# Kernel tuning notes

Measured on AMD Instinct MI355X. Metric: run time of the kernel, lower is better.

Reference implementation:

```python
import jax, jax.numpy as jnp
import numpy as np
from jax import lax

N, CIN, H, W = 4, 1024, 56, 56
CB = 256          # bottleneck channels
K = 9             # 3x3 kernel taps


def _conv(x, w, b, stride=1, padding='SAME'):
    y = lax.conv_general_dilated(x, w, (stride, stride), padding,
                                 dimension_numbers=('NCHW', 'OIHW', 'NCHW'))
    return y + b[None, :, None, None]


def _bilinear_gather(feat, ys, xs):
    # feat: [N,C,H,W]; ys, xs: [N,P] float sample coords. Zero padding outside.
    n, c, h, w = feat.shape
    y0 = jnp.floor(ys); x0 = jnp.floor(xs)
    wy1 = ys - y0; wy0 = 1.0 - wy1
    wx1 = xs - x0; wx0 = 1.0 - wx1
    flat = feat.reshape(n, c, h * w)

    def g(yi, xi):
        valid = (yi >= 0) & (yi <= h - 1) & (xi >= 0) & (xi <= w - 1)
        yc = jnp.clip(yi, 0, h - 1).astype(jnp.int32)
        xc = jnp.clip(xi, 0, w - 1).astype(jnp.int32)
        idx = (yc * w + xc)  # [N,P]
        vals = jnp.take_along_axis(flat, idx[:, None, :], axis=2)  # [N,C,P]
        return vals * valid[:, None, :].astype(feat.dtype)

    out = (g(y0, x0) * (wy0 * wx0)[:, None, :]
           + g(y0, x0 + 1) * (wy0 * wx1)[:, None, :]
           + g(y0 + 1, x0) * (wy1 * wx0)[:, None, :]
           + g(y0 + 1, x0 + 1) * (wy1 * wx1)[:, None, :])
    return out  # [N,C,P]


def _deform_conv3x3(feat, w, b, w_off, b_off):
    # DCNv1: offsets predicted by a standard 3x3 conv (18 = 2*K channels),
    # then bilinear-sample input at p + p_k + offset, accumulate with kernel w.
    n, c, h, ww = feat.shape
    off = _conv(feat, w_off, b_off)                 # [N, 2K, H, W]
    off = off.reshape(n, K, 2, h, ww)
    dy, dx = off[:, :, 0], off[:, :, 1]             # [N,K,H,W]
    ki, kj = jnp.meshgrid(jnp.arange(3), jnp.arange(3), indexing='ij')
    ky = (ki.reshape(-1) - 1).astype(feat.dtype)    # kernel dy offsets, rate=1
    kx = (kj.reshape(-1) - 1).astype(feat.dtype)
    hh = jnp.arange(h, dtype=feat.dtype)
    wc = jnp.arange(ww, dtype=feat.dtype)
    ys = hh[None, None, :, None] + ky[None, :, None, None] + dy   # [N,K,H,W]
    xs = wc[None, None, None, :] + kx[None, :, None, None] + dx
    sampled = _bilinear_gather(feat, ys.reshape(n, -1), xs.reshape(n, -1))
    sampled = sampled.reshape(n, c, K, h, ww)       # [N,C,K,H,W]
    out = jnp.einsum('nckhw,ock->nohw', sampled, w.reshape(w.shape[0], c, K))
    return out + b[None, :, None, None]


def setup_inputs() -> dict:
    key = jax.random.key(0)
    ks = jax.random.split(key, 6)
    x = jax.random.normal(ks[0], (N, CIN, H, W), dtype=jnp.float32)
    w1 = jax.random.normal(ks[1], (CB, CIN, 1, 1), dtype=jnp.float32) * 0.02
    b1 = jnp.zeros((CB,), jnp.float32)
    w_off = jax.random.normal(ks[2], (2 * K, CB, 3, 3), dtype=jnp.float32) * 0.01
    b_off = jnp.zeros((2 * K,), jnp.float32)
    w2 = jax.random.normal(ks[3], (CB, CB, 3, 3), dtype=jnp.float32) * 0.02
    b2 = jnp.zeros((CB,), jnp.float32)
    w3 = jax.random.normal(ks[4], (CIN, CB, 1, 1), dtype=jnp.float32) * 0.02
    b3 = jnp.zeros((CIN,), jnp.float32)
    return {"x": x, "w1": w1, "b1": b1, "w_off": w_off, "b_off": b_off,
            "w2": w2, "b2": b2, "w3": w3, "b3": b3}


def reference(x, w1, b1, w_off, b_off, w2, b2, w3, b3):
    # shortcut is identity (in_channels == out_channels, stride=1)
    r = jax.nn.relu(_conv(x, w1, b1))                      # conv1 1x1 + relu
    r = jax.nn.relu(_deform_conv3x3(r, w2, b2, w_off, b_off))  # deform 3x3 + relu
    r = _conv(r, w3, b3)                                   # conv3 1x1, no act
    return jax.nn.relu(x + r)
```

## Files before the change

kernel.cpp:

```cpp
#include <hip/hip_runtime.h>
#include <hip/hip_bf16.h>

#define N_   4
#define CIN  1024
#define H_   56
#define W_   56
#define HW   3136
#define CB   256
#define KK   9
#define OFFC 18

typedef __attribute__((ext_vector_type(8))) short short8;
typedef __attribute__((ext_vector_type(4))) short short4v;
typedef __attribute__((ext_vector_type(4))) float float4v;
typedef unsigned short ushort_t;

__device__ inline ushort_t bf16_rne(float f) {
    unsigned int u = __float_as_uint(f);
    unsigned int r = (u + 0x7FFFu + ((u >> 16) & 1u)) >> 16;
    return (ushort_t)r;
}
__device__ inline void split_bf16(float f, ushort_t& hi, ushort_t& lo) {
    ushort_t h = bf16_rne(f);
    float hf = __uint_as_float(((unsigned int)h) << 16);
    hi = h;
    lo = bf16_rne(f - hf);
}
__device__ inline short8 ld_frag_lds(const ushort_t* base) {
    short4v a = *(const short4v*)base;
    short4v b = *(const short4v*)(base + 4);
    return __builtin_shufflevector(a, b, 0, 1, 2, 3, 4, 5, 6, 7);
}
__device__ inline void lds_barrier() {
    asm volatile("s_waitcnt lgkmcnt(0)" ::: "memory");
    __builtin_amdgcn_s_barrier();
    __builtin_amdgcn_sched_barrier(0);
}

__global__ void __launch_bounds__(256) pack_weights_kernel(
    const float* __restrict__ w1, const float* __restrict__ w2,
    const float* __restrict__ w3, const float* __restrict__ w_off,
    ushort_t* __restrict__ w1p, ushort_t* __restrict__ w2p,
    ushort_t* __restrict__ w3p, ushort_t* __restrict__ wofp)
{
    int e = blockIdx.x * 256 + threadIdx.x;
    if (e < 256 * 1024) {
        int o = e >> 10, k = e & 1023;
        ushort_t hi, lo; split_bf16(w1[e], hi, lo);
        w1p[(size_t)(o * 2 + 0) * 1024 + k] = hi;
        w1p[(size_t)(o * 2 + 1) * 1024 + k] = lo;
        return;
    }
    e -= 256 * 1024;
    if (e < 256 * 256 * 9) {
        int o = e / 2304; int rem = e % 2304; int c = rem / 9; int k = rem % 9;
        w2p[(size_t)(k * 256 + o) * 256 + c] = bf16_rne(w2[e]);
        return;
    }
    e -= 256 * 256 * 9;
    if (e < 1024 * 256) {
        int o = e >> 8, k = e & 255;
        ushort_t hi, lo; split_bf16(w3[e], hi, lo);
        w3p[(size_t)(o * 2 + 0) * 256 + k] = hi;
        w3p[(size_t)(o * 2 + 1) * 256 + k] = lo;
        return;
    }
    e -= 1024 * 256;
    if (e < 9 * 32 * 256) {
        int k = e / (32 * 256);
        int rem = e % (32 * 256);
        int m = rem >> 8, c = rem & 255;
        float v = (m < OFFC) ? w_off[((size_t)m * 256 + c) * 9 + k] : 0.f;
        wofp[e] = bf16_rne(v);
    }
}

template <int MFRAG, bool RELU, bool RESID>
__global__ void __launch_bounds__(256, 4) conv1x1_mfma_kernel(
    const ushort_t* __restrict__ Wp,
    const float* __restrict__ Xin,
    const float* __restrict__ bias,
    const float* __restrict__ resid,
    float* __restrict__ Cout,
    int M, int Kdim)
{
    __shared__ ushort_t Bs[64][36];

    const int tid  = threadIdx.x;
    const int wave = tid >> 6;
    const int lane = tid & 63;
    const int l15  = lane & 15;
    const int quad = lane >> 4;
    const int pBase = blockIdx.x * 64;
    const int mBase = blockIdx.y * (MFRAG * 64) + wave * (MFRAG * 16);
    const int n     = blockIdx.z;
    const float* Xn = Xin + (size_t)n * Kdim * HW;

    float4v acc[MFRAG][4];
#pragma unroll
    for (int i = 0; i < MFRAG; ++i)
#pragma unroll
        for (int j = 0; j < 4; ++j) acc[i][j] = (float4v)(0.f);

    const int kk = tid >> 3;
    const int pq = (tid & 7) * 8;

    const float* src0 = &Xn[(size_t)kk * HW + pBase + pq];
    float4 c0 = *reinterpret_cast<const float4*>(src0);
    float4 c1 = *reinterpret_cast<const float4*>(src0 + 4);

    for (int k0 = 0; k0 < Kdim; k0 += 32) {
        lds_barrier();
        float vs[8] = {c0.x, c0.y, c0.z, c0.w, c1.x, c1.y, c1.z, c1.w};
#pragma unroll
        for (int j = 0; j < 8; ++j) Bs[pq + j][kk] = bf16_rne(vs[j]);

        short8 ah[MFRAG], al[MFRAG];
#pragma unroll
        for (int mt = 0; mt < MFRAG; ++mt) {
            const ushort_t* arow = Wp +
                ((size_t)(mBase + mt * 16 + l15) * 2) * Kdim + k0 + quad * 8;
            ah[mt] = *(const short8*)(arow);
            al[mt] = *(const short8*)(arow + Kdim);
        }
        if (k0 + 32 < Kdim) {
            const float* src = &Xn[(size_t)(k0 + 32 + kk) * HW + pBase + pq];
            c0 = *reinterpret_cast<const float4*>(src);
            c1 = *reinterpret_cast<const float4*>(src + 4);
        }
        lds_barrier();

        short8 bh[4];
#pragma unroll
        for (int nt = 0; nt < 4; ++nt)
            bh[nt] = ld_frag_lds(&Bs[nt * 16 + l15][quad * 8]);
        __builtin_amdgcn_s_setprio(1);
#pragma unroll
        for (int mt = 0; mt < MFRAG; ++mt)
#pragma unroll
            for (int nt = 0; nt < 4; ++nt) {
                acc[mt][nt] = __builtin_amdgcn_mfma_f32_16x16x32_bf16(
                    ah[mt], bh[nt], acc[mt][nt], 0, 0, 0);
                acc[mt][nt] = __builtin_amdgcn_mfma_f32_16x16x32_bf16(
                    al[mt], bh[nt], acc[mt][nt], 0, 0, 0);
            }
        __builtin_amdgcn_s_setprio(0);
    }

#pragma unroll
    for (int mt = 0; mt < MFRAG; ++mt)
#pragma unroll
        for (int rr = 0; rr < 4; ++rr) {
            int row = mBase + mt * 16 + quad * 4 + rr;
            float bv = bias[row];
#pragma unroll
            for (int nt = 0; nt < 4; ++nt) {
                int col = pBase + nt * 16 + l15;
                size_t idx = ((size_t)n * M + row) * HW + col;
                float v = acc[mt][nt][rr] + bv;
                if (RESID) v += resid[idx];
                if (RELU)  v = fmaxf(v, 0.f);
                Cout[idx] = v;
            }
        }
}

__global__ void __launch_bounds__(256, 2) offset_mfma_kernel(
    const float* __restrict__ r,
    const ushort_t* __restrict__ wofp,
    float* __restrict__ offp)
{
    __shared__ float win[32][174];

    const int tid  = threadIdx.x;
    const int h    = blockIdx.x;
    const int kh   = blockIdx.y;
    const int n    = blockIdx.z;
    const int wave = tid >> 6;
    const int lane = tid & 63;
    const int l15  = lane & 15;
    const int quad = lane >> 4;
    const float* rn = r + (size_t)n * CB * HW;
    const int cb0 = kh * 128;

    const int p = wave * 16 + l15;

    float4v acc[2];
    acc[0] = (float4v)(0.f);
    acc[1] = (float4v)(0.f);

    for (int cb = cb0; cb < cb0 + 128; cb += 32) {
        __syncthreads();
        for (int f = tid; f < 32 * 3 * 14; f += 256) {
            int c = f / 42, remf = f % 42, row = remf / 14, x4 = (remf % 14) * 4;
            int yg = h - 1 + row;
            float4 v = {0.f, 0.f, 0.f, 0.f};
            if (yg >= 0 && yg < H_)
                v = *reinterpret_cast<const float4*>(
                    &rn[(size_t)(cb + c) * HW + yg * W_ + x4]);
            *reinterpret_cast<float4*>(&win[c][row * 56 + x4]) = v;
        }
        __syncthreads();

        short8 ahA0, ahA1, ahB0, ahB1;
        {
            const ushort_t* a0 = wofp + (size_t)(0 * 32 + l15) * 256 + cb + quad * 8;
            ahA0 = *(const short8*)a0;
            ahA1 = *(const short8*)(a0 + 16 * 256);
        }
#pragma unroll
        for (int k = 0; k < KK; ++k) {
            if (k + 1 < KK) {
                const ushort_t* a1 = wofp +
                    (size_t)((k + 1) * 32 + l15) * 256 + cb + quad * 8;
                ahB0 = *(const short8*)a1;
                ahB1 = *(const short8*)(a1 + 16 * 256);
            }
            const int ky = k / 3;
            const int dx = (k % 3) - 1;
            int x = p + dx;
            bool pvalid = (p < 56) && (x >= 0) && (x < 56);
            int xc = min(max(x, 0), 55);
            short8 bh;
#pragma unroll
            for (int j = 0; j < 8; ++j) {
                float v = win[quad * 8 + j][ky * 56 + xc];
                bh[j] = (short)bf16_rne(pvalid ? v : 0.f);
            }
            acc[0] = __builtin_amdgcn_mfma_f32_16x16x32_bf16(
                ahA0, bh, acc[0], 0, 0, 0);
            acc[1] = __builtin_amdgcn_mfma_f32_16x16x32_bf16(
                ahA1, bh, acc[1], 0, 0, 0);
            ahA0 = ahB0; ahA1 = ahB1;
        }
    }

    if (p < 56) {
        float* base = offp + (size_t)(kh * N_ + n) * OFFC * HW;
#pragma unroll
        for (int mt = 0; mt < 2; ++mt)
#pragma unroll
            for (int rr = 0; rr < 4; ++rr) {
                int m = mt * 16 + quad * 4 + rr;
                if (m < OFFC)
                    base[(size_t)m * HW + h * W_ + p] = acc[mt][rr];
            }
    }
}

#define TPX   28
#define WROWS 5
#define WCOLS 36
#define WPOS  (WROWS * WCOLS)
#define CSTR  33
#define WITEMS (32 * WROWS * 9)
#define DBLK  (H_ * 2 * N_)
#define NCHUNK 8

__global__ void __launch_bounds__(512, 2) deform_mfma_kernel(
    const float* __restrict__ r,
    const float* __restrict__ off,
    const float* __restrict__ b_off,
    const ushort_t* __restrict__ w2p,
    const float* __restrict__ b2,
    float* __restrict__ r2)
{
    __shared__ float    win[WPOS][CSTR];
    __shared__ ushort_t Bs[2][KK][32][36];

    const int tid = threadIdx.x;
    const int bid = blockIdx.x;
    const int swz = (bid & 7) * (DBLK >> 3) + (bid >> 3);
    const int xh  = swz & 1;
    const int h   = (swz >> 1) % H_;
    const int n   = swz / (H_ * 2);
    const int xb  = xh * TPX;
    const float* rn    = r + (size_t)n * CB * HW;
    const float* offn0 = off + (size_t)n * OFFC * HW;
    const float* offn1 = off + (size_t)(N_ + n) * OFFC * HW;

    int   bi0 = 0, bi1 = 0, bi2 = 0, bi3 = 0;
    float bw0 = 0.f, bw1 = 0.f, bw2 = 0.f, bw3 = 0.f;
    int   go0 = 0, go1 = 0, go2 = 0, go3 = 0;
    bool  bfast = true;
    const bool bactive = (tid < 288);
    const int  bk = bactive ? (tid / 32) : 0;
    const int  bp = bactive ? (tid % 32) : 0;
    if (bactive && bp < TPX) {
        int pg = xb + bp;
        size_t iy = (size_t)(2 * bk) * HW + h * W_ + pg;
        size_t ix = (size_t)(2 * bk + 1) * HW + h * W_ + pg;
        float dy = offn0[iy] + offn1[iy] + b_off[2 * bk];
        float dx = offn0[ix] + offn1[ix] + b_off[2 * bk + 1];
        float ys = (float)(h + (bk / 3) - 1) + dy;
        float xs = (float)(pg + (bk % 3) - 1) + dx;
        float y0f = floorf(ys), x0f = floorf(xs);
        int y0 = (int)y0f, x0 = (int)x0f;
        float wy1 = ys - y0f, wy0 = 1.f - wy1;
        float wx1 = xs - x0f, wx0 = 1.f - wx1;
        int   wid[4]; float wg[4]; int gof[4]; bool fast = true;
#pragma unroll
        for (int u = 0; u < 2; ++u)
#pragma unroll
            for (int vv = 0; vv < 2; ++vv) {
                int yy = y0 + u, xx = x0 + vv;
                bool valid = (yy >= 0) && (yy <= 55) && (xx >= 0) && (xx <= 55);
                float wgt = valid ? (u ? wy1 : wy0) * (vv ? wx1 : wx0) : 0.f;
                int ry = yy - (h - 2);
                int rx = xx - (xb - 4);
                if (wgt != 0.f &&
                    (ry < 0 || ry >= WROWS || rx < 0 || rx >= WCOLS))
                    fast = false;
                int idx = min(max(ry, 0), WROWS - 1) * WCOLS +
                          min(max(rx, 0), WCOLS - 1);
                wid[u * 2 + vv] = idx;
                wg[u * 2 + vv]  = wgt;
                gof[u * 2 + vv] = valid ? (yy * W_ + xx) : 0;
            }
        bfast = fast;
        bi0 = wid[0]; bi1 = wid[1]; bi2 = wid[2]; bi3 = wid[3];
        bw0 = wg[0];  bw1 = wg[1];  bw2 = wg[2];  bw3 = wg[3];
        go0 = gof[0]; go1 = gof[1]; go2 = gof[2]; go3 = gof[3];
    }

    const int wave = tid >> 6;
    const int lane = tid & 63;
    const int l15  = lane & 15;
    const int quad = lane >> 4;
    const int mW   = wave * 32;

    float4v acc[2][2];
#pragma unroll
    for (int i = 0; i < 2; ++i)
#pragma unroll
        for (int j = 0; j < 2; ++j) acc[i][j] = (float4v)(0.f);

    auto wload = [&](int f, int cbg) -> float4 {
        int c = f / 45, remf = f % 45, row = remf / 9, q = remf % 9;
        int yg = min(max(h - 2 + row, 0), H_ - 1);
        int xg = xb - 4 + q * 4;
        const float* src = &rn[(size_t)(cbg + c) * HW + yg * W_];
        float4 v;
        if (xg >= 0 && xg <= W_ - 4) {
            v = *reinterpret_cast<const float4*>(src + xg);
        } else {
            v.x = src[min(max(xg + 0, 0), W_ - 1)];
            v.y = src[min(max(xg + 1, 0), W_ - 1)];
            v.z = src[min(max(xg + 2, 0), W_ - 1)];
            v.w = src[min(max(xg + 3, 0), W_ - 1)];
        }
        return v;
    };
    auto wwrite = [&](float4* pre) {
#pragma unroll
        for (int i = 0; i < 3; ++i) {
            int f = tid + 512 * i;
            if (f < WITEMS) {
                int c = f / 45, remf = f % 45, row = remf / 9, q = remf % 9;
                int pos = row * WCOLS + q * 4;
                float4 v = pre[i];
                win[pos + 0][c] = v.x;
                win[pos + 1][c] = v.y;
                win[pos + 2][c] = v.z;
                win[pos + 3][c] = v.w;
            }
        }
    };
    auto build = [&](int cbg, int pb) {
#pragma unroll
        for (int c4 = 0; c4 < 32; c4 += 4) {
            float s[4];
            if (bfast) {
#pragma unroll
                for (int j = 0; j < 4; ++j) {
                    int c = c4 + j;
                    s[j] = bw0 * win[bi0][c] + bw1 * win[bi1][c] +
                           bw2 * win[bi2][c] + bw3 * win[bi3][c];
                }
            } else {
#pragma unroll
                for (int j = 0; j < 4; ++j) {
                    const float* rc = rn + (size_t)(cbg + c4 + j) * HW;
                    s[j] = bw0 * rc[go0] + bw1 * rc[go1] +
                           bw2 * rc[go2] + bw3 * rc[go3];
                }
            }
            short4v pk;
#pragma unroll
            for (int j = 0; j < 4; ++j) pk[j] = (short)bf16_rne(s[j]);
            *(short4v*)&Bs[pb][bk][bp][c4] = pk;
        }
    };

    float4 pre[3];
#pragma unroll
    for (int i = 0; i < 3; ++i) {
        int f = tid + 512 * i;
        if (f < WITEMS) pre[i] = wload(f, 0);
    }
    wwrite(pre);
#pragma unroll
    for (int i = 0; i < 3; ++i) {
        int f = tid + 512 * i;
        if (f < WITEMS) pre[i] = wload(f, 32);
    }
    lds_barrier();
    if (bactive) build(0, 0);
    lds_barrier();

    for (int ci = 0; ci < NCHUNK; ++ci) {
        const int cb = ci * 32;
        const bool hasNext = (ci + 1 < NCHUNK);
        if (hasNext) {
            wwrite(pre);
            if (ci + 2 < NCHUNK) {
#pragma unroll
                for (int i = 0; i < 3; ++i) {
                    int f = tid + 512 * i;
                    if (f < WITEMS) pre[i] = wload(f, cb + 64);
                }
            }
            lds_barrier();
            if (bactive) build(cb + 32, (ci + 1) & 1);
        }

        const ushort_t* bsb = &Bs[ci & 1][0][0][0];
        __builtin_amdgcn_s_setprio(1);
#pragma unroll
        for (int k = 0; k < KK; ++k) {
            short8 ah[2];
#pragma unroll
            for (int mt = 0; mt < 2; ++mt) {
                const ushort_t* arow = w2p +
                    (size_t)(k * 256 + (mW + mt * 16 + l15)) * 256 +
                    cb + quad * 8;
                ah[mt] = *(const short8*)(arow);
            }
            short8 bh[2];
#pragma unroll
            for (int nt = 0; nt < 2; ++nt)
                bh[nt] = ld_frag_lds(bsb + ((size_t)k * 32 +
                         nt * 16 + l15) * 36 + quad * 8);
#pragma unroll
            for (int mt = 0; mt < 2; ++mt)
#pragma unroll
                for (int nt = 0; nt < 2; ++nt)
                    acc[mt][nt] = __builtin_amdgcn_mfma_f32_16x16x32_bf16(
                        ah[mt], bh[nt], acc[mt][nt], 0, 0, 0);
        }
        __builtin_amdgcn_s_setprio(0);
        if (hasNext) lds_barrier();
    }

#pragma unroll
    for (int mt = 0; mt < 2; ++mt)
#pragma unroll
        for (int rr = 0; rr < 4; ++rr) {
            int o = mW + mt * 16 + quad * 4 + rr;
            float bv = b2[o];
#pragma unroll
            for (int nt = 0; nt < 2; ++nt) {
                int p = nt * 16 + l15;
                if (p < TPX) {
                    float v = fmaxf(acc[mt][nt][rr] + bv, 0.f);
                    r2[((size_t)n * CB + o) * HW + h * W_ + xb + p] = v;
                }
            }
        }
}

extern "C" void kernel_launch(void* const* d_in, const int* in_sizes, int n_in,
                              void* d_out, int out_size, void* d_ws, size_t ws_size,
                              hipStream_t stream)
{
    const float* x     = (const float*)d_in[0];
    const float* w1    = (const float*)d_in[1];
    const float* b1    = (const float*)d_in[2];
    const float* w_off = (const float*)d_in[3];
    const float* b_off = (const float*)d_in[4];
    const float* w2    = (const float*)d_in[5];
    const float* b2    = (const float*)d_in[6];
    const float* w3    = (const float*)d_in[7];
    const float* b3    = (const float*)d_in[8];
    float* out = (float*)d_out;

    float* ws  = (float*)d_ws;
    float* r    = ws;
    float* r2   = r  + (size_t)N_ * CB * HW;
    float* offb = r2 + (size_t)N_ * CB * HW;
    ushort_t* w1p  = (ushort_t*)(offb + (size_t)2 * N_ * OFFC * HW);
    ushort_t* w2p  = w1p + (size_t)256 * 2 * 1024;
    ushort_t* w3p  = w2p + (size_t)9 * 256 * 256;
    ushort_t* wofp = w3p + (size_t)1024 * 2 * 256;

    {
        int total = 256 * 1024 + 256 * 256 * 9 + 1024 * 256 + 9 * 32 * 256;
        pack_weights_kernel<<<(total + 255) / 256, 256, 0, stream>>>(
            w1, w2, w3, w_off, w1p, w2p, w3p, wofp);
    }
    {
        dim3 grid(HW / 64, CB / 64, N_);
        conv1x1_mfma_kernel<1, true, false><<<grid, 256, 0, stream>>>(
            w1p, x, b1, nullptr, r, CB, CIN);
    }
    {
        dim3 grid(H_, 2, N_);
        offset_mfma_kernel<<<grid, 256, 0, stream>>>(r, wofp, offb);
    }
    {
        deform_mfma_kernel<<<DBLK, 512, 0, stream>>>(
            r, offb, b_off, w2p, b2, r2);
    }
    {
        dim3 grid(HW / 64, CIN / 128, N_);
        conv1x1_mfma_kernel<2, true, true><<<grid, 256, 0, stream>>>(
            w3p, r2, b3, x, out, CIN, CB);
    }
}
```

Baseline: 333.8 us.

## Fuse hi/lo bf16 weight split into 1x1 conv kernels and widen K tile

The 1x1 conv kernels now read fp32 weights directly and split them into bf16 hi/lo pairs in registers, so the prepack of w1 and w3 is dropped from the packing kernel. The K step per iteration doubles from 32 to 64, with a larger LDS tile and more MFMAs per barrier. conv1 moves to MFRAG=2 with half as many blocks along M, and launch bounds drop to 3 waves per SIMD. This removes a packing pass and halves the barrier count, but the weight conversion is now repeated in every block and register pressure rises.

```diff
diff --git a/kernel.cpp b/kernel.cpp
--- a/kernel.cpp
+++ b/kernel.cpp
@@ -31,6 +31,18 @@
     short4v b = *(const short4v*)(base + 4);
     return __builtin_shufflevector(a, b, 0, 1, 2, 3, 4, 5, 6, 7);
 }
+__device__ inline void cvt_hilo(const float* p, short8& hi, short8& lo) {
+    float4 a = *reinterpret_cast<const float4*>(p);
+    float4 b = *reinterpret_cast<const float4*>(p + 4);
+    float f[8] = {a.x, a.y, a.z, a.w, b.x, b.y, b.z, b.w};
+#pragma unroll
+    for (int j = 0; j < 8; ++j) {
+        ushort_t h, l;
+        split_bf16(f[j], h, l);
+        hi[j] = (short)h;
+        lo[j] = (short)l;
+    }
+}
 __device__ inline void lds_barrier() {
     asm volatile("s_waitcnt lgkmcnt(0)" ::: "memory");
     __builtin_amdgcn_s_barrier();
@@ -38,34 +50,16 @@
 }
 
 __global__ void __launch_bounds__(256) pack_weights_kernel(
-    const float* __restrict__ w1, const float* __restrict__ w2,
-    const float* __restrict__ w3, const float* __restrict__ w_off,
-    ushort_t* __restrict__ w1p, ushort_t* __restrict__ w2p,
-    ushort_t* __restrict__ w3p, ushort_t* __restrict__ wofp)
+    const float* __restrict__ w2, const float* __restrict__ w_off,
+    ushort_t* __restrict__ w2p, ushort_t* __restrict__ wofp)
 {
     int e = blockIdx.x * 256 + threadIdx.x;
-    if (e < 256 * 1024) {
-        int o = e >> 10, k = e & 1023;
-        ushort_t hi, lo; split_bf16(w1[e], hi, lo);
-        w1p[(size_t)(o * 2 + 0) * 1024 + k] = hi;
-        w1p[(size_t)(o * 2 + 1) * 1024 + k] = lo;
-        return;
-    }
-    e -= 256 * 1024;
     if (e < 256 * 256 * 9) {
         int o = e / 2304; int rem = e % 2304; int c = rem / 9; int k = rem % 9;
         w2p[(size_t)(k * 256 + o) * 256 + c] = bf16_rne(w2[e]);
         return;
     }
     e -= 256 * 256 * 9;
-    if (e < 1024 * 256) {
-        int o = e >> 8, k = e & 255;
-        ushort_t hi, lo; split_bf16(w3[e], hi, lo);
-        w3p[(size_t)(o * 2 + 0) * 256 + k] = hi;
-        w3p[(size_t)(o * 2 + 1) * 256 + k] = lo;
-        return;
-    }
-    e -= 1024 * 256;
     if (e < 9 * 32 * 256) {
         int k = e / (32 * 256);
         int rem = e % (32 * 256);
@@ -76,15 +70,15 @@
 }
 
 template <int MFRAG, bool RELU, bool RESID>
-__global__ void __launch_bounds__(256, 4) conv1x1_mfma_kernel(
-    const ushort_t* __restrict__ Wp,
+__global__ void __launch_bounds__(256, 3) conv1x1_mfma_kernel(
+    const float* __restrict__ Wfp,
     const float* __restrict__ Xin,
     const float* __restrict__ bias,
     const float* __restrict__ resid,
     float* __restrict__ Cout,
     int M, int Kdim)
 {
-    __shared__ ushort_t Bs[64][36];
+    __shared__ ushort_t Bs[64][70];
 
     const int tid  = threadIdx.x;
     const int wave = tid >> 6;
@@ -102,47 +96,63 @@
 #pragma unroll
         for (int j = 0; j < 4; ++j) acc[i][j] = (float4v)(0.f);
 
-    const int kk = tid >> 3;
-    const int pq = (tid & 7) * 8;
-
-    const float* src0 = &Xn[(size_t)kk * HW + pBase + pq];
-    float4 c0 = *reinterpret_cast<const float4*>(src0);
-    float4 c1 = *reinterpret_cast<const float4*>(src0 + 4);
-
-    for (int k0 = 0; k0 < Kdim; k0 += 32) {
+    const int kk2 = tid >> 2;
+    const int pq2 = (tid & 3) * 16;
+
+    float4 c0, c1, c2, c3;
+    {
+        const float* s = &Xn[(size_t)kk2 * HW + pBase + pq2];
+        c0 = *reinterpret_cast<const float4*>(s);
+        c1 = *reinterpret_cast<const float4*>(s + 4);
+        c2 = *reinterpret_cast<const float4*>(s + 8);
+        c3 = *reinterpret_cast<const float4*>(s + 12);
+    }
+
+    for (int k0 = 0; k0 < Kdim; k0 += 64) {
         lds_barrier();
-        float vs[8] = {c0.x, c0.y, c0.z, c0.w, c1.x, c1.y, c1.z, c1.w};
-#pragma unroll
-        for (int j = 0; j < 8; ++j) Bs[pq + j][kk] = bf16_rne(vs[j]);
-
-        short8 ah[MFRAG], al[MFRAG];
+        {
+            float vs[16] = {c0.x, c0.y, c0.z, c0.w, c1.x, c1.y, c1.z, c1.w,
+                            c2.x, c2.y, c2.z, c2.w, c3.x, c3.y, c3.z, c3.w};
+#pragma unroll
+            for (int j = 0; j < 16; ++j) Bs[pq2 + j][kk2] = bf16_rne(vs[j]);
+        }
+
+        short8 ah[MFRAG][2], al[MFRAG][2];
 #pragma unroll
         for (int mt = 0; mt < MFRAG; ++mt) {
-            const ushort_t* arow = Wp +
-                ((size_t)(mBase + mt * 16 + l15) * 2) * Kdim + k0 + quad * 8;
-            ah[mt] = *(const short8*)(arow);
-            al[mt] = *(const short8*)(arow + Kdim);
-        }
-        if (k0 + 32 < Kdim) {
-            const float* src = &Xn[(size_t)(k0 + 32 + kk) * HW + pBase + pq];
-            c0 = *reinterpret_cast<const float4*>(src);
-            c1 = *reinterpret_cast<const float4*>(src + 4);
+            const float* arow = Wfp +
+                (size_t)(mBase + mt * 16 + l15) * Kdim + k0 + quad * 8;
+            cvt_hilo(arow,      ah[mt][0], al[mt][0]);
+            cvt_hilo(arow + 32, ah[mt][1], al[mt][1]);
+        }
+        if (k0 + 64 < Kdim) {
+            const float* s = &Xn[(size_t)(k0 + 64 + kk2) * HW + pBase + pq2];
+            c0 = *reinterpret_cast<const float4*>(s);
+            c1 = *reinterpret_cast<const float4*>(s + 4);
+            c2 = *reinterpret_cast<const float4*>(s + 8);
+            c3 = *reinterpret_cast<const float4*>(s + 12);
         }
         lds_barrier();
 
-        short8 bh[4];
+        short8 bh[4][2];
 #pragma unroll
         for (int nt = 0; nt < 4; ++nt)
-            bh[nt] = ld_frag_lds(&Bs[nt * 16 + l15][quad * 8]);
+#pragma unroll
+            for (int h = 0; h < 2; ++h)
+                bh[nt][h] = ld_frag_lds(&Bs[nt * 16 + l15][h * 32 + quad * 8]);
         __builtin_amdgcn_s_setprio(1);
 #pragma unroll
         for (int mt = 0; mt < MFRAG; ++mt)
 #pragma unroll
             for (int nt = 0; nt < 4; ++nt) {
                 acc[mt][nt] = __builtin_amdgcn_mfma_f32_16x16x32_bf16(
-                    ah[mt], bh[nt], acc[mt][nt], 0, 0, 0);
+                    ah[mt][0], bh[nt][0], acc[mt][nt], 0, 0, 0);
                 acc[mt][nt] = __builtin_amdgcn_mfma_f32_16x16x32_bf16(
-                    al[mt], bh[nt], acc[mt][nt], 0, 0, 0);
+                    al[mt][0], bh[nt][0], acc[mt][nt], 0, 0, 0);
+                acc[mt][nt] = __builtin_amdgcn_mfma_f32_16x16x32_bf16(
+                    ah[mt][1], bh[nt][1], acc[mt][nt], 0, 0, 0);
+                acc[mt][nt] = __builtin_amdgcn_mfma_f32_16x16x32_bf16(
+                    al[mt][1], bh[nt][1], acc[mt][nt], 0, 0, 0);
             }
         __builtin_amdgcn_s_setprio(0);
     }
@@ -488,20 +498,18 @@
     float* r    = ws;
     float* r2   = r  + (size_t)N_ * CB * HW;
     float* offb = r2 + (size_t)N_ * CB * HW;
-    ushort_t* w1p  = (ushort_t*)(offb + (size_t)2 * N_ * OFFC * HW);
-    ushort_t* w2p  = w1p + (size_t)256 * 2 * 1024;
-    ushort_t* w3p  = w2p + (size_t)9 * 256 * 256;
-    ushort_t* wofp = w3p + (size_t)1024 * 2 * 256;
+    ushort_t* w2p  = (ushort_t*)(offb + (size_t)2 * N_ * OFFC * HW);
+    ushort_t* wofp = w2p + (size_t)9 * 256 * 256;
 
     {
-        int total = 256 * 1024 + 256 * 256 * 9 + 1024 * 256 + 9 * 32 * 256;
+        int total = 256 * 256 * 9 + 9 * 32 * 256;
         pack_weights_kernel<<<(total + 255) / 256, 256, 0, stream>>>(
-            w1, w2, w3, w_off, w1p, w2p, w3p, wofp);
+            w2, w_off, w2p, wofp);
     }
     {
-        dim3 grid(HW / 64, CB / 64, N_);
-        conv1x1_mfma_kernel<1, true, false><<<grid, 256, 0, stream>>>(
-            w1p, x, b1, nullptr, r, CB, CIN);
+        dim3 grid(HW / 64, CB / 128, N_);
+        conv1x1_mfma_kernel<2, true, false><<<grid, 256, 0, stream>>>(
+            w1, x, b1, nullptr, r, CB, CIN);
     }
     {
         dim3 grid(H_, 2, N_);
@@ -514,6 +522,6 @@
     {
         dim3 grid(HW / 64, CIN / 128, N_);
         conv1x1_mfma_kernel<2, true, true><<<grid, 256, 0, stream>>>(
-            w3p, r2, b3, x, out, CIN, CB);
-    }
-}
+            w3, r2, b3, x, out, CIN, CB);
+    }
+}
```

Result: slower. 395.9 us (+18.6%).
